# Kernel optimization log

Measured on AMD Instinct MI355X. Metric: run time of the kernel, lower is better.

Reference implementation:

```python
import jax, jax.numpy as jnp
import numpy as np

NUM_LAYERS = 3

def setup_inputs() -> dict:
    key = jax.random.key(0)
    k1, k2, k3, k4 = jax.random.split(key, 4)
    N, D, E = 100000, 128, 3200000
    x = jax.random.normal(k1, (N, D), dtype=jnp.float32)
    edge_row = jax.random.randint(k2, (E,), 0, N, dtype=jnp.int64 if jax.config.jax_enable_x64 else jnp.int32)
    edge_col = jax.random.randint(k3, (E,), 0, N, dtype=jnp.int64 if jax.config.jax_enable_x64 else jnp.int32)
    # normalized-adjacency-like positive values
    edge_val = jax.random.uniform(k4, (E,), dtype=jnp.float32)
    return {"x": x, "edge_row": edge_row, "edge_col": edge_col, "edge_val": edge_val}

def _spmm(edge_row, edge_col, edge_val, emb, num_nodes):
    # out[r] += val * emb[c]  -- sparse adjacency @ emb
    msgs = edge_val[:, None] * emb[edge_col]          # [E, D] gather + scale
    return jax.ops.segment_sum(msgs, edge_row, num_segments=num_nodes)

def reference(x, edge_row, edge_col, edge_val):
    N = x.shape[0]
    emb = x
    acc = x  # running sum over layer embeddings (layer 0 included)
    for _ in range(NUM_LAYERS):
        emb = _spmm(edge_row, edge_col, edge_val, emb, N)
        acc = acc + emb
    # mean over (num_layers + 1) stacked embeddings, without materializing the stack
    return acc / jnp.float32(NUM_LAYERS + 1)
```

## Files before the change

### kernel.cpp

```cpp
#include <hip/hip_runtime.h>

#define DIMS 128
#define RPB 64
#define CAP 3072
#define NBK_MAX 1600
#define NBINS 1024

typedef _Float16 half_t;
typedef _Float16 half2_t __attribute__((ext_vector_type(2)));

static __device__ __forceinline__ unsigned halfbits(float v) {
    half_t h = (half_t)v;
    unsigned short us;
    __builtin_memcpy(&us, &h, 2);
    return (unsigned)us;
}

__global__ void cvt_kernel(const float* __restrict__ src, half_t* __restrict__ dst, int n2) {
    int i = blockIdx.x * blockDim.x + threadIdx.x;
    if (i >= n2) return;
    float2 v = reinterpret_cast<const float2*>(src)[i];
    half2_t h;
    h.x = (half_t)v.x;
    h.y = (half_t)v.y;
    reinterpret_cast<half2_t*>(&dst[0])[i] = h;
}

__global__ __launch_bounds__(256) void binA_kernel(
    const int* __restrict__ row, const int* __restrict__ col,
    const float* __restrict__ val, int E, int nbk,
    int* __restrict__ fill, int2* __restrict__ staged) {
    __shared__ int cnt[NBK_MAX];
    __shared__ int base[NBK_MAX];
    const int t = threadIdx.x;
    const int tile0 = blockIdx.x * 8192;
    for (int j = t; j < nbk; j += 256) cnt[j] = 0;
    __syncthreads();
    for (int k = 0; k < 8; ++k) {
        int e = tile0 + (k * 256 + t) * 4;
        if (e + 3 < E) {
            int4 r4 = *reinterpret_cast<const int4*>(&row[e]);
            atomicAdd(&cnt[r4.x >> 6], 1);
            atomicAdd(&cnt[r4.y >> 6], 1);
            atomicAdd(&cnt[r4.z >> 6], 1);
            atomicAdd(&cnt[r4.w >> 6], 1);
        } else {
            for (int j = e; j < E; ++j) atomicAdd(&cnt[row[j] >> 6], 1);
        }
    }
    __syncthreads();
    for (int j = t; j < nbk; j += 256) {
        int c = cnt[j];
        base[j] = c ? atomicAdd(&fill[j], c) : 0;
        cnt[j] = 0;
    }
    __syncthreads();
    for (int k = 0; k < 8; ++k) {
        int e = tile0 + (k * 256 + t) * 4;
        int n = (e + 3 < E) ? 4 : max(0, E - e);
        if (n == 4) {
            int4 r4 = *reinterpret_cast<const int4*>(&row[e]);
            int4 c4 = *reinterpret_cast<const int4*>(&col[e]);
            float4 v4 = *reinterpret_cast<const float4*>(&val[e]);
            int rr[4] = {r4.x, r4.y, r4.z, r4.w};
            int cc[4] = {c4.x, c4.y, c4.z, c4.w};
            float vv[4] = {v4.x, v4.y, v4.z, v4.w};
#pragma unroll
            for (int j = 0; j < 4; ++j) {
                int b = rr[j] >> 6;
                int p = base[b] + atomicAdd(&cnt[b], 1);
                if (p < CAP) {
                    unsigned hb = halfbits(vv[j]);
                    int2 pk;
                    pk.x = (int)(((unsigned)(rr[j] & 63) << 26) | ((unsigned)cc[j] << 8));
                    pk.y = (int)((hb << 16) | hb);
                    staged[(size_t)b * CAP + p] = pk;
                }
            }
        } else {
            for (int j = e; j < e + n; ++j) {
                int r = row[j];
                int b = r >> 6;
                int p = base[b] + atomicAdd(&cnt[b], 1);
                if (p < CAP) {
                    unsigned hb = halfbits(val[j]);
                    int2 pk;
                    pk.x = (int)(((unsigned)(r & 63) << 26) | ((unsigned)col[j] << 8));
                    pk.y = (int)((hb << 16) | hb);
                    staged[(size_t)b * CAP + p] = pk;
                }
            }
        }
    }
}

__global__ __launch_bounds__(512) void sort_bucket(
    const int* __restrict__ fill, int2* __restrict__ staged,
    int* __restrict__ rowinfo, int N) {
    __shared__ int2 buf[CAP];
    __shared__ int2 outb[CAP];
    __shared__ int cur[NBINS];
    __shared__ int wsum[8];
    const int b = blockIdx.x;
    const int t = threadIdx.x;
    const int w = t >> 6, lane = t & 63;
    const int cnt = min(fill[b], CAP);
    int2* gb = staged + (size_t)b * CAP;

    cur[2 * t] = 0;
    cur[2 * t + 1] = 0;
    for (int i = t; i < cnt; i += 512) buf[i] = gb[i];
    __syncthreads();
    for (int i = t; i < cnt; i += 512) {
        unsigned k = (unsigned)buf[i].x;
        int key = (int)((k >> 26) << 4) | (int)((k >> 21) & 0xF);
        atomicAdd(&cur[key], 1);
    }
    __syncthreads();
    int h0 = cur[2 * t], h1 = cur[2 * t + 1];
    int s = h0 + h1;
    int v = s;
    for (int d = 1; d < 64; d <<= 1) {
        int u = __shfl_up(v, d, 64);
        if (lane >= d) v += u;
    }
    if (lane == 63) wsum[w] = v;
    __syncthreads();
    if (t < 8) {
        int ws = wsum[t];
        int vv = ws;
        for (int d = 1; d < 8; d <<= 1) {
            int u = __shfl_up(vv, d, 64);
            if (t >= d) vv += u;
        }
        wsum[t] = vv - ws;
    }
    __syncthreads();
    int excl = wsum[w] + (v - s);
    cur[2 * t] = excl;
    cur[2 * t + 1] = excl + h0;
    __syncthreads();
    if (t < RPB) {
        int start = cur[t * 16];
        int end = (t == RPB - 1) ? cnt : cur[t * 16 + 16];
        int r = b * RPB + t;
        if (r < N) rowinfo[r] = (start << 16) | end;
    }
    __syncthreads();
    for (int i = t; i < cnt; i += 512) {
        int2 pk = buf[i];
        unsigned k = (unsigned)pk.x;
        int key = (int)((k >> 26) << 4) | (int)((k >> 21) & 0xF);
        int p = atomicAdd(&cur[key], 1);
        outb[p] = pk;
    }
    __syncthreads();
    for (int i = t; i < cnt; i += 512) gb[i] = outb[i];
}

template <int MODE>
__global__ __launch_bounds__(256) void spmm_kernel(
    const half_t* __restrict__ emb_in, const int* __restrict__ rowinfo,
    const int2* __restrict__ staged, int N,
    half_t* __restrict__ emb_out, half_t* __restrict__ acc_h,
    float* __restrict__ out) {
    int r = (blockIdx.x * blockDim.x + threadIdx.x) >> 6;
    int lane = threadIdx.x & 63;
    if (r >= N) return;
    int info = rowinfo[r];
    int start = info >> 16;
    int end = info & 0xFFFF;
    const int2* eb = staged + (size_t)(r >> 6) * CAP;
    const char* tbl = reinterpret_cast<const char*>(emb_in);
    const unsigned lane4 = (unsigned)lane << 2;

    half2_t acc[8];
#pragma unroll
    for (int k = 0; k < 8; ++k) acc[k] = (half2_t)0;

    for (int base = start; base < end; base += 64) {
        const int cnt = min(64, end - base);
        int2 myE = make_int2(0, 0);
        if (base + lane < end) myE = eb[base + lane];

        int k = 0;
        for (; k + 7 < cnt; k += 8) {
            int ex[8], ey[8];
#pragma unroll
            for (int j = 0; j < 8; ++j) {
                ex[j] = __shfl(myE.x, k + j, 64);
                ey[j] = __shfl(myE.y, k + j, 64);
            }
            half2_t tv[8];
#pragma unroll
            for (int j = 0; j < 8; ++j) {
                unsigned voff = (((unsigned)ex[j]) & 0x03FFFF00u) + lane4;
                tv[j] = *reinterpret_cast<const half2_t*>(tbl + voff);
            }
#pragma unroll
            for (int j = 0; j < 8; ++j) {
                half2_t vv = __builtin_bit_cast(half2_t, ey[j]);
                acc[j] = tv[j] * vv + acc[j];
            }
        }
        for (; k < cnt; ++k) {
            int ex = __shfl(myE.x, k, 64);
            int ey = __shfl(myE.y, k, 64);
            unsigned voff = (((unsigned)ex) & 0x03FFFF00u) + lane4;
            half2_t tvs = *reinterpret_cast<const half2_t*>(tbl + voff);
            half2_t vv = __builtin_bit_cast(half2_t, ey);
            acc[0] = tvs * vv + acc[0];
        }
    }
    half2_t a01 = acc[0] + acc[1], a23 = acc[2] + acc[3];
    half2_t a45 = acc[4] + acc[5], a67 = acc[6] + acc[7];
    half2_t a = (a01 + a23) + (a45 + a67);

    size_t o = (size_t)r * DIMS + 2 * lane;
    if (MODE == 0 || MODE == 1) {
        *reinterpret_cast<half2_t*>(&emb_out[o]) = a;
    }
    if (MODE == 0) {
        half2_t xv = *reinterpret_cast<const half2_t*>(&emb_in[o]);
        *reinterpret_cast<half2_t*>(&acc_h[o]) = xv + a;
    } else if (MODE == 1) {
        half2_t cv = *reinterpret_cast<half2_t*>(&acc_h[o]);
        *reinterpret_cast<half2_t*>(&acc_h[o]) = cv + a;
    } else {
        half2_t cv = *reinterpret_cast<half2_t*>(&acc_h[o]);
        *reinterpret_cast<float2*>(&out[o]) =
            make_float2(((float)cv.x + (float)a.x) * 0.25f,
                        ((float)cv.y + (float)a.y) * 0.25f);
    }
}


extern "C" void kernel_launch(void* const* d_in, const int* in_sizes, int n_in,
                              void* d_out, int out_size, void* d_ws, size_t ws_size,
                              hipStream_t stream) {
    const float* x = (const float*)d_in[0];
    const int* erow = (const int*)d_in[1];
    const int* ecol = (const int*)d_in[2];
    const float* eval = (const float*)d_in[3];
    const int N = in_sizes[0] / DIMS;
    const int E = in_sizes[1];
    float* out = (float*)d_out;
    const int nbk = (N + RPB - 1) / RPB;

    char* ws = (char*)d_ws;
    size_t off = 0;
    auto carve = [&](size_t bytes) {
        void* p = ws + off;
        off = (off + bytes + 255) & ~(size_t)255;
        return p;
    };
    half_t* xh = (half_t*)carve((size_t)N * DIMS * sizeof(half_t));
    half_t* embB1 = (half_t*)carve((size_t)N * DIMS * sizeof(half_t));
    half_t* acc_h = (half_t*)carve((size_t)N * DIMS * sizeof(half_t));
    int2* staged = (int2*)carve((size_t)nbk * CAP * sizeof(int2));
    int* fill = (int*)carve((size_t)nbk * sizeof(int));
    int* rowinfo = (int*)carve((size_t)N * sizeof(int));
    (void)ws_size;

    hipMemsetAsync(fill, 0, (size_t)nbk * sizeof(int), stream);
    const int n2 = N * DIMS / 2;
    cvt_kernel<<<(n2 + 255) / 256, 256, 0, stream>>>(x, xh, n2);
    binA_kernel<<<(E + 8191) / 8192, 256, 0, stream>>>(erow, ecol, eval, E, nbk, fill, staged);
    sort_bucket<<<nbk, 512, 0, stream>>>(fill, staged, rowinfo, N);

    const int spmm_blocks = (N + 3) / 4;
    spmm_kernel<0><<<spmm_blocks, 256, 0, stream>>>(xh, rowinfo, staged, N, embB1, acc_h, out);
    spmm_kernel<1><<<spmm_blocks, 256, 0, stream>>>(embB1, rowinfo, staged, N, xh, acc_h, out);
    spmm_kernel<2><<<spmm_blocks, 256, 0, stream>>>(xh, rowinfo, staged, N, embB1, acc_h, out);
}
```

Baseline: 541.3 us.

## Split wavefront into four 16-lane groups gathering 16-byte rows per edge

The SpMM kernel now has each quarter-wave of 16 lanes gather a full 256-byte fp16 embedding row with 16-byte loads, so four edges are processed at once per wave instead of one edge per 4-byte-per-lane load. The partial sums from the four groups are combined with cross-lane xor shuffles, and the first 16 lanes write the results with vector stores. This is meant to cut the number of memory instructions and shuffles per edge and raise memory-level parallelism in the gather. In exchange it adds a reduction step at the end and a masked tail path that wastes some lanes when the edge count is not a multiple of 16.

```diff
diff --git a/kernel.cpp b/kernel.cpp
--- a/kernel.cpp
+++ b/kernel.cpp
@@ -15,6 +15,8 @@
     __builtin_memcpy(&us, &h, 2);
     return (unsigned)us;
 }
+static __device__ __forceinline__ half2_t h2(int b) { return __builtin_bit_cast(half2_t, b); }
+static __device__ __forceinline__ int ih(half2_t h) { return __builtin_bit_cast(int, h); }
 
 __global__ void cvt_kernel(const float* __restrict__ src, half_t* __restrict__ dst, int n2) {
     int i = blockIdx.x * blockDim.x + threadIdx.x;
@@ -164,19 +166,22 @@
     const int2* __restrict__ staged, int N,
     half_t* __restrict__ emb_out, half_t* __restrict__ acc_h,
     float* __restrict__ out) {
-    int r = (blockIdx.x * blockDim.x + threadIdx.x) >> 6;
-    int lane = threadIdx.x & 63;
+    const int r = (blockIdx.x * blockDim.x + threadIdx.x) >> 6;
+    const int lane = threadIdx.x & 63;
     if (r >= N) return;
-    int info = rowinfo[r];
-    int start = info >> 16;
-    int end = info & 0xFFFF;
+    const int info = rowinfo[r];
+    const int start = info >> 16;
+    const int end = info & 0xFFFF;
     const int2* eb = staged + (size_t)(r >> 6) * CAP;
     const char* tbl = reinterpret_cast<const char*>(emb_in);
-    const unsigned lane4 = (unsigned)lane << 2;
-
-    half2_t acc[8];
-#pragma unroll
-    for (int k = 0; k < 8; ++k) acc[k] = (half2_t)0;
+    const int g = lane >> 4;
+    const unsigned q16 = (unsigned)(lane & 15) << 4;
+
+    half2_t acc[4][4];
+#pragma unroll
+    for (int u = 0; u < 4; ++u)
+#pragma unroll
+        for (int s = 0; s < 4; ++s) acc[u][s] = (half2_t)0;
 
     for (int base = start; base < end; base += 64) {
         const int cnt = min(64, end - base);
@@ -184,53 +189,95 @@
         if (base + lane < end) myE = eb[base + lane];
 
         int k = 0;
-        for (; k + 7 < cnt; k += 8) {
-            int ex[8], ey[8];
-#pragma unroll
-            for (int j = 0; j < 8; ++j) {
-                ex[j] = __shfl(myE.x, k + j, 64);
-                ey[j] = __shfl(myE.y, k + j, 64);
-            }
-            half2_t tv[8];
-#pragma unroll
-            for (int j = 0; j < 8; ++j) {
-                unsigned voff = (((unsigned)ex[j]) & 0x03FFFF00u) + lane4;
-                tv[j] = *reinterpret_cast<const half2_t*>(tbl + voff);
-            }
-#pragma unroll
-            for (int j = 0; j < 8; ++j) {
-                half2_t vv = __builtin_bit_cast(half2_t, ey[j]);
-                acc[j] = tv[j] * vv + acc[j];
-            }
-        }
-        for (; k < cnt; ++k) {
-            int ex = __shfl(myE.x, k, 64);
-            int ey = __shfl(myE.y, k, 64);
-            unsigned voff = (((unsigned)ex) & 0x03FFFF00u) + lane4;
-            half2_t tvs = *reinterpret_cast<const half2_t*>(tbl + voff);
-            half2_t vv = __builtin_bit_cast(half2_t, ey);
-            acc[0] = tvs * vv + acc[0];
-        }
-    }
-    half2_t a01 = acc[0] + acc[1], a23 = acc[2] + acc[3];
-    half2_t a45 = acc[4] + acc[5], a67 = acc[6] + acc[7];
-    half2_t a = (a01 + a23) + (a45 + a67);
-
-    size_t o = (size_t)r * DIMS + 2 * lane;
-    if (MODE == 0 || MODE == 1) {
-        *reinterpret_cast<half2_t*>(&emb_out[o]) = a;
-    }
-    if (MODE == 0) {
-        half2_t xv = *reinterpret_cast<const half2_t*>(&emb_in[o]);
-        *reinterpret_cast<half2_t*>(&acc_h[o]) = xv + a;
-    } else if (MODE == 1) {
-        half2_t cv = *reinterpret_cast<half2_t*>(&acc_h[o]);
-        *reinterpret_cast<half2_t*>(&acc_h[o]) = cv + a;
-    } else {
-        half2_t cv = *reinterpret_cast<half2_t*>(&acc_h[o]);
-        *reinterpret_cast<float2*>(&out[o]) =
-            make_float2(((float)cv.x + (float)a.x) * 0.25f,
-                        ((float)cv.y + (float)a.y) * 0.25f);
+        for (; k + 16 <= cnt; k += 16) {
+            int ex[4], ey[4];
+#pragma unroll
+            for (int u = 0; u < 4; ++u) {
+                ex[u] = __shfl(myE.x, k + 4 * u + g, 64);
+                ey[u] = __shfl(myE.y, k + 4 * u + g, 64);
+            }
+            int4 tv[4];
+#pragma unroll
+            for (int u = 0; u < 4; ++u) {
+                unsigned voff = ((unsigned)ex[u] & 0x03FFFF00u) + q16;
+                tv[u] = *reinterpret_cast<const int4*>(tbl + voff);
+            }
+#pragma unroll
+            for (int u = 0; u < 4; ++u) {
+                half2_t vv = h2(ey[u]);
+                acc[u][0] = h2(tv[u].x) * vv + acc[u][0];
+                acc[u][1] = h2(tv[u].y) * vv + acc[u][1];
+                acc[u][2] = h2(tv[u].z) * vv + acc[u][2];
+                acc[u][3] = h2(tv[u].w) * vv + acc[u][3];
+            }
+        }
+        if (k < cnt) {
+            int ex[4], ey[4];
+#pragma unroll
+            for (int u = 0; u < 4; ++u) {
+                const int idx = k + 4 * u + g;
+                const int cl = min(idx, cnt - 1);
+                ex[u] = __shfl(myE.x, cl, 64);
+                int tmp = __shfl(myE.y, cl, 64);
+                ey[u] = (idx < cnt) ? tmp : 0;
+            }
+            int4 tv[4];
+#pragma unroll
+            for (int u = 0; u < 4; ++u) {
+                unsigned voff = ((unsigned)ex[u] & 0x03FFFF00u) + q16;
+                tv[u] = *reinterpret_cast<const int4*>(tbl + voff);
+            }
+#pragma unroll
+            for (int u = 0; u < 4; ++u) {
+                half2_t vv = h2(ey[u]);
+                acc[u][0] = h2(tv[u].x) * vv + acc[u][0];
+                acc[u][1] = h2(tv[u].y) * vv + acc[u][1];
+                acc[u][2] = h2(tv[u].z) * vv + acc[u][2];
+                acc[u][3] = h2(tv[u].w) * vv + acc[u][3];
+            }
+        }
+    }
+
+    half2_t a0 = (acc[0][0] + acc[1][0]) + (acc[2][0] + acc[3][0]);
+    half2_t a1 = (acc[0][1] + acc[1][1]) + (acc[2][1] + acc[3][1]);
+    half2_t a2 = (acc[0][2] + acc[1][2]) + (acc[2][2] + acc[3][2]);
+    half2_t a3 = (acc[0][3] + acc[1][3]) + (acc[2][3] + acc[3][3]);
+#pragma unroll
+    for (int off = 16; off < 64; off <<= 1) {
+        a0 = a0 + h2(__shfl_xor(ih(a0), off, 64));
+        a1 = a1 + h2(__shfl_xor(ih(a1), off, 64));
+        a2 = a2 + h2(__shfl_xor(ih(a2), off, 64));
+        a3 = a3 + h2(__shfl_xor(ih(a3), off, 64));
+    }
+
+    if (lane < 16) {
+        const size_t o = (size_t)r * DIMS + ((size_t)lane << 3);
+        if (MODE == 0 || MODE == 1) {
+            *reinterpret_cast<int4*>(&emb_out[o]) = make_int4(ih(a0), ih(a1), ih(a2), ih(a3));
+        }
+        if (MODE == 0) {
+            int4 xv = *reinterpret_cast<const int4*>(&emb_in[o]);
+            *reinterpret_cast<int4*>(&acc_h[o]) = make_int4(
+                ih(h2(xv.x) + a0), ih(h2(xv.y) + a1), ih(h2(xv.z) + a2), ih(h2(xv.w) + a3));
+        } else if (MODE == 1) {
+            int4 cv = *reinterpret_cast<const int4*>(&acc_h[o]);
+            *reinterpret_cast<int4*>(&acc_h[o]) = make_int4(
+                ih(h2(cv.x) + a0), ih(h2(cv.y) + a1), ih(h2(cv.z) + a2), ih(h2(cv.w) + a3));
+        } else {
+            int4 cv = *reinterpret_cast<const int4*>(&acc_h[o]);
+            half2_t c0 = h2(cv.x), c1 = h2(cv.y), c2 = h2(cv.z), c3 = h2(cv.w);
+            float4 f0 = make_float4(((float)c0.x + (float)a0.x) * 0.25f,
+                                    ((float)c0.y + (float)a0.y) * 0.25f,
+                                    ((float)c1.x + (float)a1.x) * 0.25f,
+                                    ((float)c1.y + (float)a1.y) * 0.25f);
+            float4 f1 = make_float4(((float)c2.x + (float)a2.x) * 0.25f,
+                                    ((float)c2.y + (float)a2.y) * 0.25f,
+                                    ((float)c3.x + (float)a3.x) * 0.25f,
+                                    ((float)c3.y + (float)a3.y) * 0.25f);
+            float4* po = reinterpret_cast<float4*>(&out[o]);
+            po[0] = f0;
+            po[1] = f1;
+        }
     }
 }
 
```

Measured after the change: 546.7 us. About the same (+1.0%).
